# Kernel optimization log

Measured on AMD Instinct MI355X. Metric: run time of the kernel, lower is better.

Reference implementation:

```python
import jax, jax.numpy as jnp
from jax import lax
import numpy as np

B, IN_DIM, T = 32, 40, 1000
OUT_DIM = 512          # hp.output_dim
TDNN5_DIM = 1500       # layer5 channels
STATS_DIM = 2 * TDNN5_DIM  # mean||std -> 3000
FC_HID = 512
NUM_CLASSES = 1000


def setup_inputs() -> dict:
    key = jax.random.key(0)
    ks = jax.random.split(key, 18)
    def p(k, shape, fan_in):
        return jax.random.normal(k, shape, dtype=jnp.float32) * np.float32(1.0 / np.sqrt(fan_in))
    return {
        "x":  jax.random.normal(ks[0], (B, IN_DIM, T), dtype=jnp.float32),
        # TDNN kernels: [out_ch, in_ch, width], init N(0, 1/sqrt(in_dim)) as in source
        "k1": p(ks[1], (OUT_DIM, IN_DIM, 5), IN_DIM),  "c1": p(ks[2], (OUT_DIM,), IN_DIM),
        "k2": p(ks[3], (OUT_DIM, OUT_DIM, 5), OUT_DIM), "c2": p(ks[4], (OUT_DIM,), OUT_DIM),
        "k3": p(ks[5], (OUT_DIM, OUT_DIM, 7), OUT_DIM), "c3": p(ks[6], (OUT_DIM,), OUT_DIM),
        "k4": p(ks[7], (OUT_DIM, OUT_DIM, 1), OUT_DIM), "c4": p(ks[8], (OUT_DIM,), OUT_DIM),
        "k5": p(ks[9], (TDNN5_DIM, OUT_DIM, 1), OUT_DIM), "c5": p(ks[10], (TDNN5_DIM,), OUT_DIM),
        # FullyConnected (torch Linear weights are [out, in])
        "w1": p(ks[11], (FC_HID, STATS_DIM), STATS_DIM), "d1": p(ks[12], (FC_HID,), STATS_DIM),
        "w2": p(ks[13], (OUT_DIM, FC_HID), FC_HID),      "d2": p(ks[14], (OUT_DIM,), FC_HID),
        # last_layer
        "wl": p(ks[15], (NUM_CLASSES, OUT_DIM), OUT_DIM), "dl": p(ks[16], (NUM_CLASSES,), OUT_DIM),
    }


def _tdnn(h, kernel, bias, a, b):
    """Faithful TDNN_cpu with full_context range [a..b].
    h: [B, T, C_in] -> [B, T', C_out] with ReLU.
    valid_steps = range(max(0,-a), T - max(0,b)); output[c] uses frames [c+a, c+b],
    i.e. a VALID conv over frames starting at max(a,0)."""
    ht = jnp.transpose(h, (0, 2, 1))  # [B, C, T]
    width = b - a + 1
    Tlen = ht.shape[2]
    count = Tlen - max(0, b) - max(0, -a)   # number of valid steps
    start = max(a, 0)                        # first frame used by first valid step
    hs = lax.slice_in_dim(ht, start, start + count + width - 1, axis=2)
    out = lax.conv_general_dilated(hs, kernel, window_strides=(1,), padding='VALID',
                                   dimension_numbers=('NCH', 'OIH', 'NCH'))
    out = jax.nn.relu(out + bias[None, :, None])
    return jnp.transpose(out, (0, 2, 1))  # [B, T', C_out]


def reference(x, k1, c1, k2, c2, k3, c3, k4, c4, k5, c5, w1, d1, w2, d2, wl, dl):
    h = jnp.transpose(x, (0, 2, 1))          # [B, T, IN_DIM]
    h = _tdnn(h, k1, c1, -2, 2)              # width 5
    h = _tdnn(h, k2, c2, -2, 2)              # [-2,1,2] full_context -> [-2..2]
    h = _tdnn(h, k3, c3, -3, 3)              # width 7
    h = _tdnn(h, k4, c4, 1, 1)               # width-1 conv, +1 frame shift
    h = _tdnn(h, k5, c5, 1, 1)               # -> [B, T5, 1500]
    mean = h.mean(axis=1)
    std = jnp.std(h, axis=1, ddof=1)         # torch.std is unbiased by default
    stats = jnp.concatenate([mean, std], axis=1)  # [B, 3000]
    e = jax.nn.relu(stats @ w1.T + d1)
    embedding = jax.nn.relu(e @ w2.T + d2)   # [B, 512]
    prob = embedding @ wl.T + dl             # [B, num_classes]
    return (embedding, prob)
```

## Files before the change

### kernel.cpp

```cpp
#include <hip/hip_runtime.h>
#include <hip/hip_bf16.h>

#define NB 32
#define T0_ 1000
#define IN_DIM_ 40
#define OUT_DIM_ 512
#define TDNN5_ 1500
#define T1_ 996
#define T2_ 992
#define T3_ 986
#define T4_ 985
#define T5_ 984
#define NCLS_ 1000

#define TM 128
#define TN 64
#define KB 32

typedef __attribute__((ext_vector_type(8))) short short8_t;
typedef __attribute__((ext_vector_type(4))) float float4_t;

#define GLDS16(gp, lp) __builtin_amdgcn_global_load_lds( \
    (__attribute__((address_space(1))) void*)(gp), \
    (__attribute__((address_space(3))) void*)(lp), 16, 0, 0)

__device__ __forceinline__ unsigned short f2bf(float f) {
    unsigned int u = __float_as_uint(f);
    unsigned int r = u + 0x7FFFu + ((u >> 16) & 1u);
    return (unsigned short)(r >> 16);
}
__device__ __forceinline__ float bf2f(unsigned short h) {
    return __uint_as_float((unsigned int)h << 16);
}


__global__ __launch_bounds__(256) void xsplit_k(const float* __restrict__ x,
                                                unsigned short* __restrict__ xhi,
                                                unsigned short* __restrict__ xlo) {
    int idx = blockIdx.x * 256 + threadIdx.x;
    if (idx >= NB * T0_ * IN_DIM_) return;
    int i = idx % IN_DIM_;
    int t = (idx / IN_DIM_) % T0_;
    int b = idx / (IN_DIM_ * T0_);
    float v = x[((size_t)b * IN_DIM_ + i) * T0_ + t];
    unsigned short h = f2bf(v);
    xhi[idx] = h;
    xlo[idx] = f2bf(v - bf2f(h));
}

__global__ __launch_bounds__(256) void wsplit_k(const float* __restrict__ src,
                                                unsigned short* __restrict__ whi,
                                                unsigned short* __restrict__ wlo,
                                                int N, int Npad, int K, int Kpad,
                                                int Ci, int W) {
    long total = (long)Npad * Kpad;
    long idx = (long)blockIdx.x * 256 + threadIdx.x;
    if (idx >= total) return;
    int n = (int)(idx / Kpad);
    int k = (int)(idx % Kpad);
    float v = 0.f;
    if (n < N && k < K) {
        int w = k / Ci, i = k % Ci;
        v = src[((size_t)n * Ci + i) * W + w];
    }
    unsigned short h = f2bf(v);
    whi[idx] = h;
    wlo[idx] = f2bf(v - bf2f(h));
}

__global__ __launch_bounds__(256) void zero_k(float* __restrict__ p, int n) {
    int i = blockIdx.x * 256 + threadIdx.x;
    if (i < n) p[i] = 0.f;
}

template <bool STATS>
__global__ __launch_bounds__(256, 3) void conv_mfma(
    const unsigned short* __restrict__ in_hi, const unsigned short* __restrict__ in_lo,
    const unsigned short* __restrict__ w_hi,  const unsigned short* __restrict__ w_lo,
    const float* __restrict__ bias,
    unsigned short* __restrict__ out_hi, unsigned short* __restrict__ out_lo,
    float* __restrict__ gsum, float* __restrict__ gsq,
    int GY, int M, int N, int Kpad, int Ci, int rowOff, long inB, long outB) {

    __shared__ unsigned short As_hi[TM][KB];
    __shared__ unsigned short As_lo[TM][KB];
    __shared__ unsigned short Bs_hi[TN][KB];
    __shared__ unsigned short Bs_lo[TN][KB];

    const int tid  = threadIdx.x;
    const int lane = tid & 63;
    const int wav  = tid >> 6;
    const int lr   = lane & 15;
    const int lq   = lane >> 4;

    const int bid = blockIdx.x;
    const int n0 = (bid % GY) * TN;
    const int rem = bid / GY;
    const int t0 = (rem & 7) * TM;
    const int b  = rem >> 3;

    const int sr = lane >> 2;
    const int sc = (lane & 3) * 8;
    const unsigned short* Ah = in_hi + (size_t)b * inB;
    const unsigned short* Al = in_lo + (size_t)b * inB;
    const size_t gA0 = (size_t)(t0 + rowOff + 32 * wav + sr) * Ci + sc;
    const size_t gA1 = (size_t)(t0 + rowOff + 32 * wav + 16 + sr) * Ci + sc;
    const size_t gB  = (size_t)(n0 + 16 * wav + sr) * Kpad + sc;
    unsigned short* ldsA0h = &As_hi[32 * wav][0];
    unsigned short* ldsA1h = &As_hi[32 * wav + 16][0];
    unsigned short* ldsA0l = &As_lo[32 * wav][0];
    unsigned short* ldsA1l = &As_lo[32 * wav + 16][0];
    unsigned short* ldsBh  = &Bs_hi[16 * wav][0];
    unsigned short* ldsBl  = &Bs_lo[16 * wav][0];

    float4_t acc[2][4];
    #pragma unroll
    for (int mi = 0; mi < 2; ++mi)
        #pragma unroll
        for (int nj = 0; nj < 4; ++nj) acc[mi][nj] = (float4_t)0.f;

    for (int k0 = 0; k0 < Kpad; k0 += KB) {
        __syncthreads();
        GLDS16(Ah + gA0 + k0, ldsA0h);
        GLDS16(Ah + gA1 + k0, ldsA1h);
        GLDS16(Al + gA0 + k0, ldsA0l);
        GLDS16(Al + gA1 + k0, ldsA1l);
        GLDS16(w_hi + gB + k0, ldsBh);
        GLDS16(w_lo + gB + k0, ldsBl);
        asm volatile("s_waitcnt vmcnt(0)" ::: "memory");
        __syncthreads();

        short8_t ahf[2], alf[2], bhf[4], blf[4];
        #pragma unroll
        for (int mi = 0; mi < 2; ++mi) {
            int r = wav * 32 + mi * 16 + lr;
            ahf[mi] = *(const short8_t*)&As_hi[r][lq * 8];
            alf[mi] = *(const short8_t*)&As_lo[r][lq * 8];
        }
        #pragma unroll
        for (int nj = 0; nj < 4; ++nj) {
            bhf[nj] = *(const short8_t*)&Bs_hi[nj * 16 + lr][lq * 8];
            blf[nj] = *(const short8_t*)&Bs_lo[nj * 16 + lr][lq * 8];
        }
        #pragma unroll
        for (int mi = 0; mi < 2; ++mi)
            #pragma unroll
            for (int nj = 0; nj < 4; ++nj) {
                acc[mi][nj] = __builtin_amdgcn_mfma_f32_16x16x32_bf16(ahf[mi], bhf[nj], acc[mi][nj], 0, 0, 0);
                acc[mi][nj] = __builtin_amdgcn_mfma_f32_16x16x32_bf16(alf[mi], bhf[nj], acc[mi][nj], 0, 0, 0);
                acc[mi][nj] = __builtin_amdgcn_mfma_f32_16x16x32_bf16(ahf[mi], blf[nj], acc[mi][nj], 0, 0, 0);
            }
    }

    if (!STATS) {
        #pragma unroll
        for (int mi = 0; mi < 2; ++mi)
            #pragma unroll
            for (int rr = 0; rr < 4; ++rr) {
                int r = t0 + wav * 32 + mi * 16 + lq * 4 + rr;
                if (r < M) {
                    #pragma unroll
                    for (int nj = 0; nj < 4; ++nj) {
                        int n = n0 + nj * 16 + lr;
                        float v = fmaxf(acc[mi][nj][rr] + bias[n], 0.f);
                        unsigned short h = f2bf(v);
                        size_t o = (size_t)b * outB + (size_t)r * N + n;
                        out_hi[o] = h;
                        out_lo[o] = f2bf(v - bf2f(h));
                    }
                }
            }
    } else {
        float cs[4] = {0.f, 0.f, 0.f, 0.f}, cq[4] = {0.f, 0.f, 0.f, 0.f};
        #pragma unroll
        for (int mi = 0; mi < 2; ++mi)
            #pragma unroll
            for (int rr = 0; rr < 4; ++rr) {
                int r = t0 + wav * 32 + mi * 16 + lq * 4 + rr;
                if (r < M) {
                    #pragma unroll
                    for (int nj = 0; nj < 4; ++nj) {
                        int n = n0 + nj * 16 + lr;
                        if (n < N) {
                            float v = fmaxf(acc[mi][nj][rr] + bias[n], 0.f);
                            cs[nj] += v;
                            cq[nj] += v * v;
                        }
                    }
                }
            }
        #pragma unroll
        for (int nj = 0; nj < 4; ++nj) {
            cs[nj] += __shfl_xor(cs[nj], 16);
            cs[nj] += __shfl_xor(cs[nj], 32);
            cq[nj] += __shfl_xor(cq[nj], 16);
            cq[nj] += __shfl_xor(cq[nj], 32);
            int n = n0 + nj * 16 + lr;
            if (lq == 0 && n < N) {
                atomicAdd(&gsum[(size_t)b * N + n], cs[nj]);
                atomicAdd(&gsq[(size_t)b * N + n], cq[nj]);
            }
        }
    }
}

#define AROWS 272
template <int TAPS, bool STATS>
__global__ __launch_bounds__(256, 3) void conv_tap(
    const unsigned short* __restrict__ in_hi, const unsigned short* __restrict__ in_lo,
    const unsigned short* __restrict__ w_hi,  const unsigned short* __restrict__ w_lo,
    const float* __restrict__ bias,
    unsigned short* __restrict__ out_hi, unsigned short* __restrict__ out_lo,
    float* __restrict__ gsum, float* __restrict__ gsq,
    int GY, int M, int N, int rowOff, long inB, long outB) {

    __shared__ unsigned short Ah_s[AROWS * 32];
    __shared__ unsigned short Al_s[AROWS * 32];
    __shared__ unsigned short Bh_s[TN * 32];
    __shared__ unsigned short Bl_s[TN * 32];

    const int tid  = threadIdx.x;
    const int lane = tid & 63;
    const int wav  = tid >> 6;
    const int lr   = lane & 15;
    const int lq   = lane >> 4;
    const int KSTR = TAPS * 512;

    const int bid = blockIdx.x;
    const int n0 = (bid % GY) * TN;
    const int rem = bid / GY;
    const int t0 = (rem & 3) * 256;
    const int b  = rem >> 2;

    const int arow = tid >> 2;
    const int acol = (tid & 3) * 8;
    const unsigned short* Agh = in_hi + (size_t)b * inB + (size_t)(t0 + rowOff) * 512;
    const unsigned short* Agl = in_lo + (size_t)b * inB + (size_t)(t0 + rowOff) * 512;
    const size_t bsrc0 = (size_t)(n0 + (tid >> 2)) * KSTR + acol;
    unsigned short* dB_h = Bh_s + wav * 512;
    unsigned short* dB_l = Bl_s + wav * 512;

    float4_t acc[4][4];
    #pragma unroll
    for (int mi = 0; mi < 4; ++mi)
        #pragma unroll
        for (int nj = 0; nj < 4; ++nj) acc[mi][nj] = (float4_t)0.f;

    for (int c32 = 0; c32 < 16; ++c32) {
        const int cc = c32 * 32;
        #pragma unroll
        for (int q = 0; q < 4; ++q) {
            size_t aoff = (size_t)(q * 64 + arow) * 512 + cc + acol;
            GLDS16(Agh + aoff, Ah_s + (q * 256 + wav * 64) * 8);
            GLDS16(Agl + aoff, Al_s + (q * 256 + wav * 64) * 8);
        }
        if (wav == 0) {
            size_t aoff = (size_t)(256 + (lane >> 2)) * 512 + cc + (lane & 3) * 8;
            GLDS16(Agh + aoff, Ah_s + 1024 * 8);
            GLDS16(Agl + aoff, Al_s + 1024 * 8);
        }
        #pragma unroll
        for (int w = 0; w < TAPS; ++w) {
            GLDS16(w_hi + bsrc0 + w * 512 + cc, dB_h);
            GLDS16(w_lo + bsrc0 + w * 512 + cc, dB_l);
            asm volatile("s_waitcnt vmcnt(0)" ::: "memory");
            __syncthreads();
            short8_t ahf[4], alf[4], bhf[4], blf[4];
            #pragma unroll
            for (int mi = 0; mi < 4; ++mi) {
                int r = wav * 64 + mi * 16 + lr + w;
                ahf[mi] = *(const short8_t*)&Ah_s[r * 32 + lq * 8];
                alf[mi] = *(const short8_t*)&Al_s[r * 32 + lq * 8];
            }
            #pragma unroll
            for (int nj = 0; nj < 4; ++nj) {
                bhf[nj] = *(const short8_t*)&Bh_s[(nj * 16 + lr) * 32 + lq * 8];
                blf[nj] = *(const short8_t*)&Bl_s[(nj * 16 + lr) * 32 + lq * 8];
            }
            #pragma unroll
            for (int mi = 0; mi < 4; ++mi)
                #pragma unroll
                for (int nj = 0; nj < 4; ++nj) {
                    acc[mi][nj] = __builtin_amdgcn_mfma_f32_16x16x32_bf16(ahf[mi], bhf[nj], acc[mi][nj], 0, 0, 0);
                    acc[mi][nj] = __builtin_amdgcn_mfma_f32_16x16x32_bf16(alf[mi], bhf[nj], acc[mi][nj], 0, 0, 0);
                    acc[mi][nj] = __builtin_amdgcn_mfma_f32_16x16x32_bf16(ahf[mi], blf[nj], acc[mi][nj], 0, 0, 0);
                }
            __syncthreads();
        }
    }

    if (!STATS) {
        #pragma unroll
        for (int mi = 0; mi < 4; ++mi)
            #pragma unroll
            for (int rr = 0; rr < 4; ++rr) {
                int r = t0 + wav * 64 + mi * 16 + lq * 4 + rr;
                if (r < M) {
                    #pragma unroll
                    for (int nj = 0; nj < 4; ++nj) {
                        int n = n0 + nj * 16 + lr;
                        float v = fmaxf(acc[mi][nj][rr] + bias[n], 0.f);
                        unsigned short h = f2bf(v);
                        size_t o = (size_t)b * outB + (size_t)r * N + n;
                        out_hi[o] = h;
                        out_lo[o] = f2bf(v - bf2f(h));
                    }
                }
            }
    } else {
        float cs[4] = {0.f, 0.f, 0.f, 0.f}, cq[4] = {0.f, 0.f, 0.f, 0.f};
        #pragma unroll
        for (int mi = 0; mi < 4; ++mi)
            #pragma unroll
            for (int rr = 0; rr < 4; ++rr) {
                int r = t0 + wav * 64 + mi * 16 + lq * 4 + rr;
                if (r < M) {
                    #pragma unroll
                    for (int nj = 0; nj < 4; ++nj) {
                        int n = n0 + nj * 16 + lr;
                        if (n < N) {
                            float v = fmaxf(acc[mi][nj][rr] + bias[n], 0.f);
                            cs[nj] += v;
                            cq[nj] += v * v;
                        }
                    }
                }
            }
        #pragma unroll
        for (int nj = 0; nj < 4; ++nj) {
            cs[nj] += __shfl_xor(cs[nj], 16);
            cs[nj] += __shfl_xor(cs[nj], 32);
            cq[nj] += __shfl_xor(cq[nj], 16);
            cq[nj] += __shfl_xor(cq[nj], 32);
            int n = n0 + nj * 16 + lr;
            if (lq == 0 && n < N) {
                atomicAdd(&gsum[(size_t)b * N + n], cs[nj]);
                atomicAdd(&gsq[(size_t)b * N + n], cq[nj]);
            }
        }
    }
}

__global__ __launch_bounds__(256) void stats_fin_k(const float* __restrict__ sum,
                                                   const float* __restrict__ sq,
                                                   float* __restrict__ stats) {
    int idx = blockIdx.x * 256 + threadIdx.x;
    if (idx >= NB * TDNN5_) return;
    int b = idx / TDNN5_, c = idx % TDNN5_;
    float s = sum[idx], q = sq[idx];
    float n = (float)T5_;
    float mean = s / n;
    float var = (q - s * s / n) / (n - 1.f);
    stats[(size_t)b * (2 * TDNN5_) + c] = mean;
    stats[(size_t)b * (2 * TDNN5_) + TDNN5_ + c] = sqrtf(fmaxf(var, 0.f));
}

__global__ __launch_bounds__(256) void fc_wave(const float* __restrict__ in,
                                               const float* __restrict__ w,
                                               const float* __restrict__ bias,
                                               float* __restrict__ out,
                                               int Bn, int N, int K4, int doRelu) {
    int wid = blockIdx.x * 4 + (threadIdx.x >> 6);
    int lane = threadIdx.x & 63;
    int b = wid / N, o = wid % N;
    if (b >= Bn) return;
    const float4* xi = (const float4*)(in + (size_t)b * K4 * 4);
    const float4* wi = (const float4*)(w + (size_t)o * K4 * 4);
    float acc = 0.f;
    for (int k = lane; k < K4; k += 64) {
        float4 xv = xi[k], wv = wi[k];
        acc += xv.x * wv.x + xv.y * wv.y + xv.z * wv.z + xv.w * wv.w;
    }
    #pragma unroll
    for (int off = 32; off > 0; off >>= 1) acc += __shfl_down(acc, off);
    if (lane == 0) {
        acc += bias[o];
        if (doRelu) acc = fmaxf(acc, 0.f);
        out[(size_t)b * N + o] = acc;
    }
}

extern "C" void kernel_launch(void* const* d_in, const int* in_sizes, int n_in,
                              void* d_out, int out_size, void* d_ws, size_t ws_size,
                              hipStream_t stream) {
    const float* x  = (const float*)d_in[0];
    const float* k1 = (const float*)d_in[1];  const float* c1 = (const float*)d_in[2];
    const float* k2 = (const float*)d_in[3];  const float* c2 = (const float*)d_in[4];
    const float* k3 = (const float*)d_in[5];  const float* c3 = (const float*)d_in[6];
    const float* k4 = (const float*)d_in[7];  const float* c4 = (const float*)d_in[8];
    const float* k5 = (const float*)d_in[9];  const float* c5 = (const float*)d_in[10];
    const float* w1 = (const float*)d_in[11]; const float* d1 = (const float*)d_in[12];
    const float* w2 = (const float*)d_in[13]; const float* d2 = (const float*)d_in[14];
    const float* wl = (const float*)d_in[15]; const float* dl = (const float*)d_in[16];

    size_t off = 0;
    auto alloc = [&](size_t bytes) { size_t o = off; off += (bytes + 255) & ~(size_t)255; return o; };
    const size_t ACT_ELEMS = (size_t)NB * T1_ * OUT_DIM_ + 32768;
    const size_t oXHI = alloc((size_t)NB * T0_ * IN_DIM_ * 2 + 8192);
    const size_t oXLO = alloc((size_t)NB * T0_ * IN_DIM_ * 2 + 8192);
    const size_t oW1H = alloc((size_t)512 * 224 * 2 + 256);
    const size_t oW1L = alloc((size_t)512 * 224 * 2 + 256);
    const size_t oW2H = alloc((size_t)512 * 2560 * 2 + 256);
    const size_t oW2L = alloc((size_t)512 * 2560 * 2 + 256);
    const size_t oW3H = alloc((size_t)512 * 3584 * 2 + 256);
    const size_t oW3L = alloc((size_t)512 * 3584 * 2 + 256);
    const size_t oW4H = alloc((size_t)512 * 512 * 2 + 256);
    const size_t oW4L = alloc((size_t)512 * 512 * 2 + 256);
    const size_t oW5H = alloc((size_t)1536 * 512 * 2 + 256);
    const size_t oW5L = alloc((size_t)1536 * 512 * 2 + 256);
    const size_t oBAH = alloc(ACT_ELEMS * 2);
    const size_t oBAL = alloc(ACT_ELEMS * 2);
    const size_t oBBH = alloc(ACT_ELEMS * 2);
    const size_t oBBL = alloc(ACT_ELEMS * 2);
    const size_t oSUM = alloc((size_t)NB * TDNN5_ * 4);
    const size_t oSQ  = alloc((size_t)NB * TDNN5_ * 4);
    const size_t oST  = alloc((size_t)NB * 2 * TDNN5_ * 4);
    const size_t oE   = alloc((size_t)NB * 512 * 4);
    if (ws_size < off) return;

    char* W = (char*)d_ws;
    unsigned short* xhi = (unsigned short*)(W + oXHI);
    unsigned short* xlo = (unsigned short*)(W + oXLO);
    unsigned short* w1h = (unsigned short*)(W + oW1H);
    unsigned short* w1l = (unsigned short*)(W + oW1L);
    unsigned short* w2h = (unsigned short*)(W + oW2H);
    unsigned short* w2l = (unsigned short*)(W + oW2L);
    unsigned short* w3h = (unsigned short*)(W + oW3H);
    unsigned short* w3l = (unsigned short*)(W + oW3L);
    unsigned short* w4h = (unsigned short*)(W + oW4H);
    unsigned short* w4l = (unsigned short*)(W + oW4L);
    unsigned short* w5h = (unsigned short*)(W + oW5H);
    unsigned short* w5l = (unsigned short*)(W + oW5L);
    unsigned short* bah = (unsigned short*)(W + oBAH);
    unsigned short* bal = (unsigned short*)(W + oBAL);
    unsigned short* bbh = (unsigned short*)(W + oBBH);
    unsigned short* bbl = (unsigned short*)(W + oBBL);
    float* gsum  = (float*)(W + oSUM);
    float* gsq   = (float*)(W + oSQ);
    float* stats = (float*)(W + oST);
    float* evec  = (float*)(W + oE);
    float* emb  = (float*)d_out;
    float* prob = (float*)d_out + NB * 512;

    dim3 blk(256);

    xsplit_k<<<(NB * T0_ * IN_DIM_ + 255) / 256, blk, 0, stream>>>(x, xhi, xlo);
    wsplit_k<<<(512 * 224 + 255) / 256, blk, 0, stream>>>(k1, w1h, w1l, 512, 512, 200, 224, IN_DIM_, 5);
    wsplit_k<<<(512 * 2560 + 255) / 256, blk, 0, stream>>>(k2, w2h, w2l, 512, 512, 2560, 2560, 512, 5);
    wsplit_k<<<(512 * 3584 + 255) / 256, blk, 0, stream>>>(k3, w3h, w3l, 512, 512, 3584, 3584, 512, 7);
    wsplit_k<<<(512 * 512 + 255) / 256, blk, 0, stream>>>(k4, w4h, w4l, 512, 512, 512, 512, 512, 1);
    wsplit_k<<<(1536 * 512 + 255) / 256, blk, 0, stream>>>(k5, w5h, w5l, 1500, 1536, 512, 512, 512, 1);
    zero_k<<<(2 * NB * TDNN5_ + 255) / 256, blk, 0, stream>>>(gsum, 2 * NB * TDNN5_);

    conv_mfma<false><<<dim3(8 * 8 * NB), blk, 0, stream>>>(
        xhi, xlo, w1h, w1l, c1, bah, bal, nullptr, nullptr,
        8, T1_, 512, 224, IN_DIM_, 0, (long)T0_ * IN_DIM_, (long)T1_ * 512);
    conv_tap<5, false><<<dim3(4 * 8 * NB), blk, 0, stream>>>(
        bah, bal, w2h, w2l, c2, bbh, bbl, nullptr, nullptr,
        8, T2_, 512, 0, (long)T1_ * 512, (long)T2_ * 512);
    conv_tap<7, false><<<dim3(4 * 8 * NB), blk, 0, stream>>>(
        bbh, bbl, w3h, w3l, c3, bah, bal, nullptr, nullptr,
        8, T3_, 512, 0, (long)T2_ * 512, (long)T3_ * 512);
    conv_tap<1, false><<<dim3(4 * 8 * NB), blk, 0, stream>>>(
        bah, bal, w4h, w4l, c4, bbh, bbl, nullptr, nullptr,
        8, T4_, 512, 1, (long)T3_ * 512, (long)T4_ * 512);
    conv_tap<1, true><<<dim3(4 * 24 * NB), blk, 0, stream>>>(
        bbh, bbl, w5h, w5l, c5, nullptr, nullptr, gsum, gsq,
        24, T5_, TDNN5_, 1, (long)T4_ * 512, 0);

    stats_fin_k<<<(NB * TDNN5_ + 255) / 256, blk, 0, stream>>>(gsum, gsq, stats);

    fc_wave<<<(NB * 512) / 4, blk, 0, stream>>>(stats, w1, d1, evec, NB, 512, 3000 / 4, 1);
    fc_wave<<<(NB * 512) / 4, blk, 0, stream>>>(evec, w2, d2, emb, NB, 512, 512 / 4, 1);
    fc_wave<<<(NB * NCLS_) / 4, blk, 0, stream>>>(emb, wl, dl, prob, NB, NCLS_, 512 / 4, 0);
}
```

Measured before the change: 1.027 ms.

## Double-buffer weight tiles in tap conv and fuse prep kernels into one launch

The tap-convolution kernel now double-buffers the weight tile in LDS. It prefetches the next tap or channel chunk's weights while MFMAs run on the current one, and issues the next activation chunk load after the last tap's fragment reads. Manual vmcnt/lgkmcnt waits and raw barriers replace the per-tap full wait plus two syncthreads, so global-load latency can overlap compute. Separately, the x split, five weight splits and the zeroing kernel are merged into one launch to cut launch overhead. The hand-counted vmcnt values and the extra tail load every wave now issues (previously only wave 0) risk ordering or race bugs if the counts are wrong.

```diff
diff --git a/kernel.cpp b/kernel.cpp
--- a/kernel.cpp
+++ b/kernel.cpp
@@ -33,29 +33,18 @@
     return __uint_as_float((unsigned int)h << 16);
 }
 
-
-__global__ __launch_bounds__(256) void xsplit_k(const float* __restrict__ x,
-                                                unsigned short* __restrict__ xhi,
-                                                unsigned short* __restrict__ xlo) {
-    int idx = blockIdx.x * 256 + threadIdx.x;
-    if (idx >= NB * T0_ * IN_DIM_) return;
-    int i = idx % IN_DIM_;
-    int t = (idx / IN_DIM_) % T0_;
-    int b = idx / (IN_DIM_ * T0_);
-    float v = x[((size_t)b * IN_DIM_ + i) * T0_ + t];
-    unsigned short h = f2bf(v);
-    xhi[idx] = h;
-    xlo[idx] = f2bf(v - bf2f(h));
-}
-
-__global__ __launch_bounds__(256) void wsplit_k(const float* __restrict__ src,
-                                                unsigned short* __restrict__ whi,
-                                                unsigned short* __restrict__ wlo,
-                                                int N, int Npad, int K, int Kpad,
-                                                int Ci, int W) {
-    long total = (long)Npad * Kpad;
-    long idx = (long)blockIdx.x * 256 + threadIdx.x;
-    if (idx >= total) return;
+#define S0E 1280000L
+#define S1E 1394688L
+#define S2E 2705408L
+#define S3E 4540416L
+#define S4E 4802560L
+#define S5E 5588992L
+#define S6E 5684992L
+__device__ __forceinline__ void wsplit_one(const float* __restrict__ src,
+                                           unsigned short* __restrict__ whi,
+                                           unsigned short* __restrict__ wlo,
+                                           long idx, int N, int K, int Kpad,
+                                           int Ci, int W) {
     int n = (int)(idx / Kpad);
     int k = (int)(idx % Kpad);
     float v = 0.f;
@@ -68,9 +57,40 @@
     wlo[idx] = f2bf(v - bf2f(h));
 }
 
-__global__ __launch_bounds__(256) void zero_k(float* __restrict__ p, int n) {
-    int i = blockIdx.x * 256 + threadIdx.x;
-    if (i < n) p[i] = 0.f;
+__global__ __launch_bounds__(256) void prep_all(
+    const float* __restrict__ x,
+    const float* __restrict__ k1, const float* __restrict__ k2,
+    const float* __restrict__ k3, const float* __restrict__ k4,
+    const float* __restrict__ k5,
+    unsigned short* __restrict__ xhi, unsigned short* __restrict__ xlo,
+    unsigned short* __restrict__ w1h, unsigned short* __restrict__ w1l,
+    unsigned short* __restrict__ w2h, unsigned short* __restrict__ w2l,
+    unsigned short* __restrict__ w3h, unsigned short* __restrict__ w3l,
+    unsigned short* __restrict__ w4h, unsigned short* __restrict__ w4l,
+    unsigned short* __restrict__ w5h, unsigned short* __restrict__ w5l,
+    float* __restrict__ gsum) {
+    long idx = (long)blockIdx.x * 256 + threadIdx.x;
+    if (idx < S0E) {
+        int i = (int)(idx % IN_DIM_);
+        int t = (int)((idx / IN_DIM_) % T0_);
+        int b = (int)(idx / (IN_DIM_ * T0_));
+        float v = x[((size_t)b * IN_DIM_ + i) * T0_ + t];
+        unsigned short h = f2bf(v);
+        xhi[idx] = h;
+        xlo[idx] = f2bf(v - bf2f(h));
+    } else if (idx < S1E) {
+        wsplit_one(k1, w1h, w1l, idx - S0E, 512, 200, 224, IN_DIM_, 5);
+    } else if (idx < S2E) {
+        wsplit_one(k2, w2h, w2l, idx - S1E, 512, 2560, 2560, 512, 5);
+    } else if (idx < S3E) {
+        wsplit_one(k3, w3h, w3l, idx - S2E, 512, 3584, 3584, 512, 7);
+    } else if (idx < S4E) {
+        wsplit_one(k4, w4h, w4l, idx - S3E, 512, 512, 512, 512, 1);
+    } else if (idx < S5E) {
+        wsplit_one(k5, w5h, w5l, idx - S4E, 1500, 512, 512, 512, 1);
+    } else if (idx < S6E) {
+        gsum[idx - S5E] = 0.f;
+    }
 }
 
 template <bool STATS>
@@ -206,7 +226,7 @@
 
 #define AROWS 272
 template <int TAPS, bool STATS>
-__global__ __launch_bounds__(256, 3) void conv_tap(
+__global__ __launch_bounds__(256, 3) void conv_pipe(
     const unsigned short* __restrict__ in_hi, const unsigned short* __restrict__ in_lo,
     const unsigned short* __restrict__ w_hi,  const unsigned short* __restrict__ w_lo,
     const float* __restrict__ bias,
@@ -216,8 +236,8 @@
 
     __shared__ unsigned short Ah_s[AROWS * 32];
     __shared__ unsigned short Al_s[AROWS * 32];
-    __shared__ unsigned short Bh_s[TN * 32];
-    __shared__ unsigned short Bl_s[TN * 32];
+    __shared__ unsigned short Bh_s[2][TN * 32];
+    __shared__ unsigned short Bl_s[2][TN * 32];
 
     const int tid  = threadIdx.x;
     const int lane = tid & 63;
@@ -237,16 +257,8 @@
     const unsigned short* Agh = in_hi + (size_t)b * inB + (size_t)(t0 + rowOff) * 512;
     const unsigned short* Agl = in_lo + (size_t)b * inB + (size_t)(t0 + rowOff) * 512;
     const size_t bsrc0 = (size_t)(n0 + (tid >> 2)) * KSTR + acol;
-    unsigned short* dB_h = Bh_s + wav * 512;
-    unsigned short* dB_l = Bl_s + wav * 512;
-
-    float4_t acc[4][4];
-    #pragma unroll
-    for (int mi = 0; mi < 4; ++mi)
-        #pragma unroll
-        for (int nj = 0; nj < 4; ++nj) acc[mi][nj] = (float4_t)0.f;
-
-    for (int c32 = 0; c32 < 16; ++c32) {
+
+    auto stageA = [&](int c32) {
         const int cc = c32 * 32;
         #pragma unroll
         for (int q = 0; q < 4; ++q) {
@@ -254,17 +266,42 @@
             GLDS16(Agh + aoff, Ah_s + (q * 256 + wav * 64) * 8);
             GLDS16(Agl + aoff, Al_s + (q * 256 + wav * 64) * 8);
         }
-        if (wav == 0) {
-            size_t aoff = (size_t)(256 + (lane >> 2)) * 512 + cc + (lane & 3) * 8;
-            GLDS16(Agh + aoff, Ah_s + 1024 * 8);
-            GLDS16(Agl + aoff, Al_s + 1024 * 8);
-        }
+        size_t toff = (size_t)(256 + (lane >> 2)) * 512 + cc + (lane & 3) * 8;
+        GLDS16(Agh + toff, Ah_s + 1024 * 8);
+        GLDS16(Agl + toff, Al_s + 1024 * 8);
+    };
+    auto stageB = [&](int c32, int w, int buf) {
+        size_t src = bsrc0 + (size_t)w * 512 + c32 * 32;
+        GLDS16(w_hi + src, &Bh_s[buf][wav * 512]);
+        GLDS16(w_lo + src, &Bl_s[buf][wav * 512]);
+    };
+
+    float4_t acc[4][4];
+    #pragma unroll
+    for (int mi = 0; mi < 4; ++mi)
+        #pragma unroll
+        for (int nj = 0; nj < 4; ++nj) acc[mi][nj] = (float4_t)0.f;
+
+    stageA(0);
+    stageB(0, 0, 0);
+    int cur = 0;
+
+    for (int c32 = 0; c32 < 16; ++c32) {
         #pragma unroll
         for (int w = 0; w < TAPS; ++w) {
-            GLDS16(w_hi + bsrc0 + w * 512 + cc, dB_h);
-            GLDS16(w_lo + bsrc0 + w * 512 + cc, dB_l);
-            asm volatile("s_waitcnt vmcnt(0)" ::: "memory");
-            __syncthreads();
+            const bool first = (w == 0);
+            const bool last  = (w == TAPS - 1);
+            const bool fin   = last && (c32 == 15);
+            if (!fin) {
+                int nc = last ? c32 + 1 : c32;
+                int nw = last ? 0 : w + 1;
+                stageB(nc, nw, cur ^ 1);
+            }
+            if (first) {
+                if (fin) asm volatile("s_waitcnt vmcnt(0)" ::: "memory");
+                else     asm volatile("s_waitcnt vmcnt(2)" ::: "memory");
+                __builtin_amdgcn_s_barrier();
+            }
             short8_t ahf[4], alf[4], bhf[4], blf[4];
             #pragma unroll
             for (int mi = 0; mi < 4; ++mi) {
@@ -274,8 +311,14 @@
             }
             #pragma unroll
             for (int nj = 0; nj < 4; ++nj) {
-                bhf[nj] = *(const short8_t*)&Bh_s[(nj * 16 + lr) * 32 + lq * 8];
-                blf[nj] = *(const short8_t*)&Bl_s[(nj * 16 + lr) * 32 + lq * 8];
+                bhf[nj] = *(const short8_t*)&Bh_s[cur][(nj * 16 + lr) * 32 + lq * 8];
+                blf[nj] = *(const short8_t*)&Bl_s[cur][(nj * 16 + lr) * 32 + lq * 8];
+            }
+            if (last && c32 < 15) {
+                asm volatile("s_waitcnt lgkmcnt(0)" ::: "memory");
+                __builtin_amdgcn_sched_barrier(0);
+                __builtin_amdgcn_s_barrier();
+                stageA(c32 + 1);
             }
             #pragma unroll
             for (int mi = 0; mi < 4; ++mi)
@@ -285,7 +328,12 @@
                     acc[mi][nj] = __builtin_amdgcn_mfma_f32_16x16x32_bf16(alf[mi], bhf[nj], acc[mi][nj], 0, 0, 0);
                     acc[mi][nj] = __builtin_amdgcn_mfma_f32_16x16x32_bf16(ahf[mi], blf[nj], acc[mi][nj], 0, 0, 0);
                 }
-            __syncthreads();
+            if (!fin) {
+                if (last && c32 < 15) asm volatile("s_waitcnt vmcnt(10)" ::: "memory");
+                else                  asm volatile("s_waitcnt vmcnt(0)"  ::: "memory");
+                __builtin_amdgcn_s_barrier();
+            }
+            cur ^= 1;
         }
     }
 
@@ -444,27 +492,23 @@
 
     dim3 blk(256);
 
-    xsplit_k<<<(NB * T0_ * IN_DIM_ + 255) / 256, blk, 0, stream>>>(x, xhi, xlo);
-    wsplit_k<<<(512 * 224 + 255) / 256, blk, 0, stream>>>(k1, w1h, w1l, 512, 512, 200, 224, IN_DIM_, 5);
-    wsplit_k<<<(512 * 2560 + 255) / 256, blk, 0, stream>>>(k2, w2h, w2l, 512, 512, 2560, 2560, 512, 5);
-    wsplit_k<<<(512 * 3584 + 255) / 256, blk, 0, stream>>>(k3, w3h, w3l, 512, 512, 3584, 3584, 512, 7);
-    wsplit_k<<<(512 * 512 + 255) / 256, blk, 0, stream>>>(k4, w4h, w4l, 512, 512, 512, 512, 512, 1);
-    wsplit_k<<<(1536 * 512 + 255) / 256, blk, 0, stream>>>(k5, w5h, w5l, 1500, 1536, 512, 512, 512, 1);
-    zero_k<<<(2 * NB * TDNN5_ + 255) / 256, blk, 0, stream>>>(gsum, 2 * NB * TDNN5_);
+    prep_all<<<(S6E + 255) / 256, blk, 0, stream>>>(
+        x, k1, k2, k3, k4, k5, xhi, xlo,
+        w1h, w1l, w2h, w2l, w3h, w3l, w4h, w4l, w5h, w5l, gsum);
 
     conv_mfma<false><<<dim3(8 * 8 * NB), blk, 0, stream>>>(
         xhi, xlo, w1h, w1l, c1, bah, bal, nullptr, nullptr,
         8, T1_, 512, 224, IN_DIM_, 0, (long)T0_ * IN_DIM_, (long)T1_ * 512);
-    conv_tap<5, false><<<dim3(4 * 8 * NB), blk, 0, stream>>>(
+    conv_pipe<5, false><<<dim3(4 * 8 * NB), blk, 0, stream>>>(
         bah, bal, w2h, w2l, c2, bbh, bbl, nullptr, nullptr,
         8, T2_, 512, 0, (long)T1_ * 512, (long)T2_ * 512);
-    conv_tap<7, false><<<dim3(4 * 8 * NB), blk, 0, stream>>>(
+    conv_pipe<7, false><<<dim3(4 * 8 * NB), blk, 0, stream>>>(
         bbh, bbl, w3h, w3l, c3, bah, bal, nullptr, nullptr,
         8, T3_, 512, 0, (long)T2_ * 512, (long)T3_ * 512);
-    conv_tap<1, false><<<dim3(4 * 8 * NB), blk, 0, stream>>>(
+    conv_pipe<1, false><<<dim3(4 * 8 * NB), blk, 0, stream>>>(
         bah, bal, w4h, w4l, c4, bbh, bbl, nullptr, nullptr,
         8, T4_, 512, 1, (long)T3_ * 512, (long)T4_ * 512);
-    conv_tap<1, true><<<dim3(4 * 24 * NB), blk, 0, stream>>>(
+    conv_pipe<1, true><<<dim3(4 * 24 * NB), blk, 0, stream>>>(
         bbh, bbl, w5h, w5l, c5, nullptr, nullptr, gsum, gsq,
         24, T5_, TDNN5_, 1, (long)T4_ * 512, 0);
 
```

New measurement: 1.178 ms. 1.15x slower.
